# Optimization experiments

Measured on AMD Instinct MI355X. Metric: run time of the kernel, lower is better.

Reference implementation:

```python
import jax, jax.numpy as jnp
import numpy as np

NEG_SLOPE = 0.2  # neg_slope init kwarg


def _segment_softmax(logits, seg, n):
    # numerically stable softmax over edges grouped by destination node
    m = jax.ops.segment_max(logits, seg, num_segments=n)          # [N,H]
    e = jnp.exp(logits - m[seg])                                   # [E,H]
    s = jax.ops.segment_sum(e, seg, num_segments=n)                # [N,H]
    return e / (s[seg] + 1e-16)


def _gat_conv(x, src, dst, W, att_src, att_dst, b, n):
    # PyG GATConv (add_self_loops already applied to src/dst), dropout off (eval)
    H, C = att_src.shape
    h = (x @ W).reshape(n, H, C)                                   # [N,H,C]
    a_src = jnp.einsum('nhc,hc->nh', h, att_src)                   # [N,H]
    a_dst = jnp.einsum('nhc,hc->nh', h, att_dst)                   # [N,H]
    logits = jax.nn.leaky_relu(a_src[src] + a_dst[dst], NEG_SLOPE)  # [E,H]
    alpha = _segment_softmax(logits, dst, n)                       # [E,H]
    msg = h[src] * alpha[:, :, None]                               # [E,H,C]
    out = jax.ops.segment_sum(msg, dst, num_segments=n)            # [N,H,C]
    return out.reshape(n, H * C) + b


def setup_inputs() -> dict:
    key = jax.random.key(0)
    ks = jax.random.split(key, 11)
    NU, NI = 10000, 100000
    N = NU + NI
    E = 1_000_000
    IN, HID, HEADS, OUT = 64, 64, 4, 64
    s = 0.1
    return {
        'edge_index': jax.random.randint(ks[0], (2, E), 0, N, dtype=jnp.int64)
            if jax.config.jax_enable_x64 else jax.random.randint(ks[0], (2, E), 0, N),
        'emb_user': jax.random.normal(ks[1], (NU, IN), jnp.float32) * s,
        'emb_item': jax.random.normal(ks[2], (NI, IN), jnp.float32) * s,
        'W1': jax.random.normal(ks[3], (IN, HEADS * HID), jnp.float32) * s,
        'att_src1': jax.random.normal(ks[4], (HEADS, HID), jnp.float32) * s,
        'att_dst1': jax.random.normal(ks[5], (HEADS, HID), jnp.float32) * s,
        'b1': jnp.zeros((HEADS * HID,), jnp.float32),
        'W2': jax.random.normal(ks[6], (HEADS * HID, OUT), jnp.float32) * s,
        'att_src2': jax.random.normal(ks[7], (1, OUT), jnp.float32) * s,
        'att_dst2': jax.random.normal(ks[8], (1, OUT), jnp.float32) * s,
        'b2': jnp.zeros((OUT,), jnp.float32),
    }


def reference(edge_index, emb_user, emb_item, W1, att_src1, att_dst1, b1,
              W2, att_src2, att_dst2, b2):
    NU = emb_user.shape[0]
    N = NU + emb_item.shape[0]
    x = jnp.concatenate([emb_user, emb_item], axis=0)              # [N,IN]
    # GATConv adds self-loops by default
    loops = jnp.arange(N, dtype=edge_index.dtype)
    src = jnp.concatenate([edge_index[0], loops])
    dst = jnp.concatenate([edge_index[1], loops])
    # dropout layers are identity in eval mode
    x = _gat_conv(x, src, dst, W1, att_src1, att_dst1, b1, N)      # [N,HEADS*HID]
    x = jax.nn.elu(x)
    x = _gat_conv(x, src, dst, W2, att_src2, att_dst2, b2, N)      # [N,OUT]
    return x[:NU], x[NU:]
```

## Files before the change

kernel.cpp:

```cpp
#include <hip/hip_runtime.h>
#include <math.h>


typedef float f32x4 __attribute__((ext_vector_type(4)));
typedef short s16x8 __attribute__((ext_vector_type(8)));

#define CHUNK 4096
#define CAPB 6400
#define PADM 1536
#define CAPT (CAPB + PADM)
#define G2PAD 264
#define SMASK 131071

static __device__ __forceinline__ short f2bf(float f) {
    unsigned u = __builtin_bit_cast(unsigned, f);
    u = (u + 0x7fff + ((u >> 16) & 1)) >> 16;
    return (short)u;
}
static __device__ __forceinline__ float bf2f(unsigned short u) {
    unsigned v = ((unsigned)u) << 16;
    return __builtin_bit_cast(float, v);
}


__global__ __launch_bounds__(256) void bin_kernel(
    const int* __restrict__ ei, int E, int ET, int* __restrict__ acur,
    unsigned long long* __restrict__ staging) {
    __shared__ unsigned long long eds[CHUNK];
    __shared__ int cnt[256], delta[256], cur[256];
    int t = threadIdx.x;
    cnt[t] = 0;
    __syncthreads();
    int c0 = blockIdx.x * CHUNK;
#pragma unroll
    for (int i = t; i < CHUNK; i += 256) {
        int e = c0 + i;
        unsigned long long v = ~0ull;
        if (e < ET) {
            int s, d;
            if (e < E) { s = ei[e]; d = ei[E + e]; } else { s = e - E; d = e - E; }
            v = ((unsigned long long)(unsigned)d << 32) | (unsigned)s;
            atomicAdd(&cnt[d >> 9], 1);
        }
        eds[i] = v;
    }
    __syncthreads();
    if (t < 64) {
        int loc[4], run = 0;
#pragma unroll
        for (int j = 0; j < 4; ++j) { int v = cnt[t * 4 + j]; loc[j] = run; run += v; }
        int inc = run;
#pragma unroll
        for (int off = 1; off < 64; off <<= 1) {
            int u = __shfl_up(inc, off);
            if (t >= off) inc += u;
        }
        int excl = inc - run;
#pragma unroll
        for (int j = 0; j < 4; ++j) {
            int b = t * 4 + j;
            int lofs = excl + loc[j];
            int c = cnt[b];
            int g = (c > 0) ? atomicAdd(&acur[b], c) : 0;
            delta[b] = b * CAPB + g - lofs;
            cur[b] = lofs;
        }
    }
    __syncthreads();
    for (int i = t; i < CHUNK; i += 256) {
        unsigned long long v = eds[i];
        if (v == ~0ull) continue;
        int b = (int)(v >> 32) >> 9;
        int p = atomicAdd(&cur[b], 1);
        int idx = delta[b] + p;
        if (idx < (b + 1) * CAPB) staging[idx] = v;
    }
}

__global__ __launch_bounds__(256) void bucket_scan_kernel(
    const int* __restrict__ acur, int* __restrict__ bbase, int NB) {
    __shared__ int sc[256];
    int t = threadIdx.x;
    int v = 0;
    if (t < NB) {
        int c = min(acur[t], CAPB);
        v = ((c + 3) & ~3) + PADM;
    }
    sc[t] = v;
    __syncthreads();
    if (t == 0) {
        int run = 0;
        for (int i = 0; i < NB; ++i) { int x = sc[i]; sc[i] = run; run += x; }
    }
    __syncthreads();
    if (t < NB) bbase[t] = sc[t];
}

__global__ __launch_bounds__(256) void bucket_build_kernel(
    const unsigned long long* __restrict__ staging, const int* __restrict__ acur,
    const int* __restrict__ bbase, const float* __restrict__ as1e,
    const float* __restrict__ ad1e, int* __restrict__ offs, int* __restrict__ ends,
    int* __restrict__ csr, int* __restrict__ dstA, float* __restrict__ wts1T,
    int N, int ETp, int NB) {
    __shared__ int src_s[CAPT];
    __shared__ unsigned short ln_s[CAPT];
    __shared__ float adl[512 * 8];
    __shared__ int cnt[512];
    __shared__ int lofs[512];
    __shared__ int tot4_s;
    int b = blockIdx.x;
    int t = threadIdx.x;
    int n0 = b << 9;
    int nn = min(512, N - n0);
    int tot = min(acur[b], CAPB);
    for (int i = t; i < nn * 8; i += 256) adl[i] = ad1e[(size_t)n0 * 8 + i];
    for (int i = t; i < 512; i += 256) cnt[i] = 0;
    for (int i = t; i < CAPT; i += 256) src_s[i] = -1;
    __syncthreads();
    const unsigned long long* sp = staging + (size_t)b * CAPB;
    for (int i = t; i < tot; i += 256)
        atomicAdd(&cnt[(int)(sp[i] >> 32) - n0], 1);
    __syncthreads();
    if (t < 64) {
        int loc[8];
        int run = 0;
#pragma unroll
        for (int j = 0; j < 8; ++j) {
            int v = (cnt[t * 8 + j] + 3) & ~3;
            loc[j] = run;
            run += v;
        }
        int inc = run;
#pragma unroll
        for (int off = 1; off < 64; off <<= 1) {
            int u = __shfl_up(inc, off);
            if (t >= off) inc += u;
        }
        int excl = inc - run;
#pragma unroll
        for (int j = 0; j < 8; ++j) lofs[t * 8 + j] = excl + loc[j];
        if (t == 63) tot4_s = inc;
    }
    __syncthreads();
    int base = bbase[b];
    int tot4 = tot4_s;
    for (int i = t; i < nn; i += 256) {
        int beg = base + lofs[i];
        offs[n0 + i] = beg;
        ends[n0 + i] = beg + ((cnt[i] + 3) & ~3);
    }
    if (b == NB - 1 && t == 0) offs[N] = base + tot4;
    __syncthreads();
    for (int i = t; i < 512; i += 256) cnt[i] = 0;
    __syncthreads();
    for (int i = t; i < tot; i += 256) {
        unsigned long long v = sp[i];
        int s = (int)(v & 0xffffffffu);
        int ln = (int)(v >> 32) - n0;
        int p = lofs[ln] + atomicAdd(&cnt[ln], 1);
        src_s[p] = s;
        ln_s[p] = (unsigned short)ln;
    }
    __syncthreads();
    for (int i = t; i < tot4; i += 256) {
        int s = src_s[i];
        if (s < 0) {
            csr[base + i] = 0;
            dstA[base + i] = -1;
            wts1T[(size_t)0 * ETp + base + i] = 0.f;
            wts1T[(size_t)1 * ETp + base + i] = 0.f;
            wts1T[(size_t)2 * ETp + base + i] = 0.f;
            wts1T[(size_t)3 * ETp + base + i] = 0.f;
        } else {
            int ln = ln_s[i];
            csr[base + i] = s;
            dstA[base + i] = n0 + ln;
            const float4* ap = reinterpret_cast<const float4*>(as1e + (size_t)s * 8);
            float4 a0 = ap[0], a1 = ap[1];
            const float* dl = adl + ln * 8;
            float wA, wB;
            wA = a0.x * dl[0]; wB = a0.y * dl[1];
            wts1T[(size_t)0 * ETp + base + i] = (wA >= 1.f) ? wA : wB;
            wA = a0.z * dl[2]; wB = a0.w * dl[3];
            wts1T[(size_t)1 * ETp + base + i] = (wA >= 1.f) ? wA : wB;
            wA = a1.x * dl[4]; wB = a1.y * dl[5];
            wts1T[(size_t)2 * ETp + base + i] = (wA >= 1.f) ? wA : wB;
            wA = a1.z * dl[6]; wB = a1.w * dl[7];
            wts1T[(size_t)3 * ETp + base + i] = (wA >= 1.f) ? wA : wB;
        }
    }
}

__global__ void edge_w2_kernel(const int* __restrict__ csr,
                               const int* __restrict__ dstA,
                               const float* __restrict__ as2e,
                               const float* __restrict__ ad2e,
                               float* __restrict__ wts2, int ETp, int N) {
    int p = blockIdx.x * blockDim.x + threadIdx.x;
    if (p >= ETp) return;
    int d = dstA[p];
    int s = csr[p];
    if ((unsigned)d >= (unsigned)N || (unsigned)s >= (unsigned)N) {
        wts2[p] = 0.f;
        return;
    }
    float2 ae = *reinterpret_cast<const float2*>(as2e + (size_t)s * 2);
    float2 de = *reinterpret_cast<const float2*>(ad2e + (size_t)d * 2);
    float wA = ae.x * de.x, wB = ae.y * de.y;
    wts2[p] = (wA >= 1.f) ? wA : wB;
}

__global__ void prep_attv_kernel(const float* __restrict__ W1,
                                 const float* __restrict__ attS1,
                                 const float* __restrict__ attD1,
                                 const float* __restrict__ W2,
                                 const float* __restrict__ attS2,
                                 const float* __restrict__ attD2,
                                 float* __restrict__ attv1s, float* __restrict__ attv1d,
                                 float* __restrict__ attv2s, float* __restrict__ attv2d) {
    int t = threadIdx.x;
    {
        int k = t >> 2, h = t & 3;
        float ss = 0.f, sd = 0.f;
        for (int c = 0; c < 64; ++c) {
            float w = W1[k * 256 + h * 64 + c];
            ss += w * attS1[h * 64 + c];
            sd += w * attD1[h * 64 + c];
        }
        attv1s[k * 4 + h] = ss;
        attv1d[k * 4 + h] = sd;
    }
    {
        float ss = 0.f, sd = 0.f;
        for (int c = 0; c < 64; ++c) {
            float w = W2[t * 64 + c];
            ss += w * attS2[c];
            sd += w * attD2[c];
        }
        attv2s[t] = ss;
        attv2d[t] = sd;
    }
}

__global__ __launch_bounds__(256) void cast_att_kernel(
    const float* __restrict__ xu, const float* __restrict__ xi, int NU, int N,
    const float* __restrict__ attv1s, const float* __restrict__ attv1d,
    unsigned short* __restrict__ xb, float* __restrict__ as1e,
    float* __restrict__ ad1e) {
    int t = threadIdx.x;
    int wv = t >> 6, l = t & 63, l15 = l & 15, lg = l >> 4;

    s16x8 Bfr[2];
#pragma unroll
    for (int ks = 0; ks < 2; ++ks) {
        s16x8 f;
#pragma unroll
        for (int j = 0; j < 8; ++j) {
            int k = ks * 32 + lg * 8 + j;
            float v = 0.f;
            if (l15 < 4) v = attv1s[k * 4 + l15];
            else if (l15 < 8) v = attv1d[k * 4 + (l15 - 4)];
            f[j] = f2bf(v);
        }
        Bfr[ks] = f;
    }

    int ntile = (N + 15) >> 4;
    int wid = blockIdx.x * 4 + wv;
    int stride = gridDim.x * 4;
    for (int tile = wid; tile < ntile; tile += stride) {
        int rbase = tile * 16;
        int arow = rbase + l15;
        bool valid = (arow < N);
        if (!valid) arow = N - 1;
        const float* xp = (arow < NU) ? (xu + (size_t)arow * 64)
                                      : (xi + (size_t)(arow - NU) * 64);
        s16x8 Afr[2];
#pragma unroll
        for (int ks = 0; ks < 2; ++ks) {
            const float4* p = reinterpret_cast<const float4*>(xp + ks * 32 + lg * 8);
            float4 v0 = p[0];
            float4 v1 = p[1];
            s16x8 f;
            f[0] = f2bf(v0.x); f[1] = f2bf(v0.y); f[2] = f2bf(v0.z); f[3] = f2bf(v0.w);
            f[4] = f2bf(v1.x); f[5] = f2bf(v1.y); f[6] = f2bf(v1.z); f[7] = f2bf(v1.w);
            Afr[ks] = f;
            if (valid)
                *reinterpret_cast<s16x8*>(xb + (size_t)arow * 64 + ks * 32 + lg * 8) = f;
        }
        f32x4 acc = (f32x4){0.f, 0.f, 0.f, 0.f};
        acc = __builtin_amdgcn_mfma_f32_16x16x32_bf16(Afr[0], Bfr[0], acc, 0, 0, 0);
        acc = __builtin_amdgcn_mfma_f32_16x16x32_bf16(Afr[1], Bfr[1], acc, 0, 0, 0);
        if (l15 < 8) {
            float* dst = (l15 < 4) ? as1e : ad1e;
            int h = l15 & 3;
#pragma unroll
            for (int i = 0; i < 4; ++i) {
                int r = rbase + lg * 4 + i;
                if (r < N) {
                    float s = acc[i];
                    dst[(size_t)r * 8 + h * 2 + 0] = __expf(s);
                    dst[(size_t)r * 8 + h * 2 + 1] = __expf(0.2f * s);
                }
            }
        }
    }
}

__global__ __launch_bounds__(256) void agg1_kernel(
    const unsigned short* __restrict__ xb, const float* __restrict__ wts1T,
    const int* __restrict__ offs, const int* __restrict__ ends,
    const int* __restrict__ csr, unsigned short* __restrict__ yb, int N, int ETp) {
    int wv = threadIdx.x >> 6, lane = threadIdx.x & 63;
    int n = __builtin_amdgcn_readfirstlane(blockIdx.x * 4 + wv);
    if (n >= N) return;
    int h = lane >> 4, c4 = (lane & 15) * 4;
    int beg = offs[n], end = ends[n];
    const float* wp = wts1T + (size_t)h * ETp;
    float ss = 0.f, a0 = 0.f, a1 = 0.f, a2 = 0.f, a3 = 0.f;

    f32x4 w0, w1, w2;
    ushort4 r0[4], r1[4], r2[4];

    if (end - beg <= 64) {
        int ci = beg + lane;
        if (ci >= end) ci = beg;
        int csrv = csr[ci] & SMASK;

#define A1F_LOAD(W, R, O)                                                         \
    {                                                                             \
        W = *reinterpret_cast<const f32x4*>(wp + (O));                            \
        _Pragma("unroll") for (int j = 0; j < 4; ++j) {                           \
            int sj = __shfl(csrv, (O) - beg + j);                                 \
            R[j] = *reinterpret_cast<const ushort4*>(xb + (size_t)sj * 64 + c4);  \
        }                                                                         \
    }
#define A1_PROC(W, R)                                                            \
    {                                                                            \
        _Pragma("unroll") for (int j = 0; j < 4; ++j) {                          \
            float w = W[j];                                                      \
            ss += w;                                                             \
            a0 += w * bf2f(R[j].x);                                              \
            a1 += w * bf2f(R[j].y);                                              \
            a2 += w * bf2f(R[j].z);                                              \
            a3 += w * bf2f(R[j].w);                                              \
        }                                                                        \
    }
        A1F_LOAD(w0, r0, beg)
        if (beg + 4 < end) {
            A1F_LOAD(w1, r1, beg + 4)
            int o = beg;
            while (true) {
                if (o + 8 < end) A1F_LOAD(w2, r2, o + 8)
                A1_PROC(w0, r0)
                o += 4; if (o >= end) break;
                if (o + 8 < end) A1F_LOAD(w0, r0, o + 8)
                A1_PROC(w1, r1)
                o += 4; if (o >= end) break;
                if (o + 8 < end) A1F_LOAD(w1, r1, o + 8)
                A1_PROC(w2, r2)
                o += 4; if (o >= end) break;
            }
        } else {
            A1_PROC(w0, r0)
        }
#undef A1F_LOAD
    } else {
#define A1_LOAD(W, R, O)                                                          \
    {                                                                             \
        W = *reinterpret_cast<const f32x4*>(wp + (O));                            \
        _Pragma("unroll") for (int j = 0; j < 4; ++j) {                           \
            int sj = __builtin_amdgcn_readfirstlane(csr[(O) + j]) & SMASK;        \
            R[j] = *reinterpret_cast<const ushort4*>(xb + (size_t)sj * 64 + c4);  \
        }                                                                         \
    }
        A1_LOAD(w0, r0, beg)
        A1_LOAD(w1, r1, beg + 4)
        int o = beg;
        while (true) {
            if (o + 8 < end) A1_LOAD(w2, r2, o + 8)
            A1_PROC(w0, r0)
            o += 4; if (o >= end) break;
            if (o + 8 < end) A1_LOAD(w0, r0, o + 8)
            A1_PROC(w1, r1)
            o += 4; if (o >= end) break;
            if (o + 8 < end) A1_LOAD(w1, r1, o + 8)
            A1_PROC(w2, r2)
            o += 4; if (o >= end) break;
        }
#undef A1_LOAD
#undef A1_PROC
    }
    float inv = 1.f / (ss + 1e-16f);
    ushort4 ov;
    ov.x = (unsigned short)f2bf(a0 * inv);
    ov.y = (unsigned short)f2bf(a1 * inv);
    ov.z = (unsigned short)f2bf(a2 * inv);
    ov.w = (unsigned short)f2bf(a3 * inv);
    *reinterpret_cast<ushort4*>(yb + (size_t)n * 256 + h * 64 + c4) = ov;
}

__global__ __launch_bounds__(256) void gemm_mid_mfma(
    const unsigned short* __restrict__ yb, int N, const float* __restrict__ W1,
    const float* __restrict__ b1, const float* __restrict__ attv2s,
    const float* __restrict__ attv2d, unsigned short* __restrict__ x2,
    float* __restrict__ as2e, float* __restrict__ ad2e) {
    __shared__ float part_s[16][4];
    __shared__ float part_d[16][4];
    int t = threadIdx.x;
    int wv = t >> 6;
    int l = t & 63;
    int l15 = l & 15;
    int lg = l >> 4;

    s16x8 Bfr[4][2];
#pragma unroll
    for (int c = 0; c < 4; ++c)
#pragma unroll
        for (int ks = 0; ks < 2; ++ks) {
            s16x8 f;
#pragma unroll
            for (int j = 0; j < 8; ++j)
                f[j] = f2bf(W1[(size_t)(ks * 32 + lg * 8 + j) * 256 + (wv * 4 + c) * 16 + l15]);
            Bfr[c][ks] = f;
        }
    float bv[4], avs[4], avd[4];
#pragma unroll
    for (int c = 0; c < 4; ++c) {
        int col = (wv * 4 + c) * 16 + l15;
        bv[c] = b1[col];
        avs[c] = attv2s[col];
        avd[c] = attv2d[col];
    }

    int ntile = (N + 15) >> 4;
    for (int tile = blockIdx.x; tile < ntile; tile += gridDim.x) {
        int rbase = tile * 16;
        int arow = rbase + l15;
        if (arow >= N) arow = N - 1;
        const unsigned short* yp = yb + (size_t)arow * 256 + wv * 64;
        s16x8 Afr0 = *reinterpret_cast<const s16x8*>(yp + lg * 8);
        s16x8 Afr1 = *reinterpret_cast<const s16x8*>(yp + 32 + lg * 8);
        f32x4 acc[4];
#pragma unroll
        for (int c = 0; c < 4; ++c) acc[c] = (f32x4){0.f, 0.f, 0.f, 0.f};
#pragma unroll
        for (int c = 0; c < 4; ++c) {
            acc[c] = __builtin_amdgcn_mfma_f32_16x16x32_bf16(Afr0, Bfr[c][0], acc[c], 0, 0, 0);
            acc[c] = __builtin_amdgcn_mfma_f32_16x16x32_bf16(Afr1, Bfr[c][1], acc[c], 0, 0, 0);
        }
        int r0 = rbase + lg * 4;
        float rs[4] = {0.f, 0.f, 0.f, 0.f};
        float rd[4] = {0.f, 0.f, 0.f, 0.f};
#pragma unroll
        for (int c = 0; c < 4; ++c) {
            int col = (wv * 4 + c) * 16 + l15;
#pragma unroll
            for (int i = 0; i < 4; ++i) {
                float v = acc[c][i] + bv[c];
                v = (v > 0.f) ? v : __expf(v) - 1.f;
                rs[i] += v * avs[c];
                rd[i] += v * avd[c];
                int r = r0 + i;
                if (r < N)
                    x2[(size_t)r * 256 + col] = (unsigned short)f2bf(v);
            }
        }
#pragma unroll
        for (int i = 0; i < 4; ++i) {
#pragma unroll
            for (int msk = 8; msk; msk >>= 1) {
                rs[i] += __shfl_xor(rs[i], msk);
                rd[i] += __shfl_xor(rd[i], msk);
            }
            if (l15 == 0) {
                part_s[lg * 4 + i][wv] = rs[i];
                part_d[lg * 4 + i][wv] = rd[i];
            }
        }
        __syncthreads();
        if (t < 16) {
            int r = rbase + t;
            if (r < N) {
                float s = part_s[t][0] + part_s[t][1] + part_s[t][2] + part_s[t][3];
                float d = part_d[t][0] + part_d[t][1] + part_d[t][2] + part_d[t][3];
                as2e[(size_t)r * 2 + 0] = __expf(s);
                as2e[(size_t)r * 2 + 1] = __expf(0.2f * s);
                ad2e[(size_t)r * 2 + 0] = __expf(d);
                ad2e[(size_t)r * 2 + 1] = __expf(0.2f * d);
            }
        }
        __syncthreads();
    }
}

__global__ __launch_bounds__(256) void gemm2_mfma(
    const unsigned short* __restrict__ x2, int N, const float* __restrict__ W2,
    unsigned short* __restrict__ h2) {
    __shared__ unsigned short at[16 * G2PAD];
    int t = threadIdx.x;
    int wv = t >> 6;
    int l = t & 63;
    int l15 = l & 15;
    int lg = l >> 4;

    s16x8 Bfr[8];
#pragma unroll
    for (int ks = 0; ks < 8; ++ks) {
        s16x8 f;
#pragma unroll
        for (int j = 0; j < 8; ++j)
            f[j] = f2bf(W2[(size_t)(ks * 32 + lg * 8 + j) * 64 + wv * 16 + l15]);
        Bfr[ks] = f;
    }

    int ntile = (N + 15) >> 4;
    for (int tile = blockIdx.x; tile < ntile; tile += gridDim.x) {
        int rbase = tile * 16;
        __syncthreads();
#pragma unroll
        for (int k = 0; k < 2; ++k) {
            int i = t * 2 + k;
            int row = i >> 5, c8 = i & 31;
            int r = rbase + row;
            if (r >= N) r = N - 1;
            *reinterpret_cast<uint4*>(at + row * G2PAD + c8 * 8) =
                *reinterpret_cast<const uint4*>(x2 + (size_t)r * 256 + c8 * 8);
        }
        __syncthreads();
        f32x4 acc = (f32x4){0.f, 0.f, 0.f, 0.f};
#pragma unroll
        for (int ks = 0; ks < 8; ++ks) {
            s16x8 Afr = *reinterpret_cast<const s16x8*>(at + l15 * G2PAD + ks * 32 + lg * 8);
            acc = __builtin_amdgcn_mfma_f32_16x16x32_bf16(Afr, Bfr[ks], acc, 0, 0, 0);
        }
        int r0 = rbase + lg * 4;
#pragma unroll
        for (int i = 0; i < 4; ++i) {
            int r = r0 + i;
            if (r < N)
                h2[(size_t)r * 64 + wv * 16 + l15] = (unsigned short)f2bf(acc[i]);
        }
    }
}

__global__ __launch_bounds__(256) void agg2_kernel(
    const unsigned short* __restrict__ h2, const float* __restrict__ wts2,
    const int* __restrict__ offs, const int* __restrict__ ends,
    const int* __restrict__ csr, const float* __restrict__ b2,
    float* __restrict__ out, int N) {
    int wv = threadIdx.x >> 6, lane = threadIdx.x & 63;
    int n = __builtin_amdgcn_readfirstlane(blockIdx.x * 4 + wv);
    if (n >= N) return;
    int beg = offs[n], end = ends[n];
    float ss = 0.f, acc = 0.f;

    f32x4 w0, w1, w2;
    unsigned short r0[4], r1[4], r2[4];

    if (end - beg <= 64) {
        int ci = beg + lane;
        if (ci >= end) ci = beg;
        int csrv = csr[ci] & SMASK;

#define A2F_LOAD(W, R, O)                                                  \
    {                                                                      \
        W = *reinterpret_cast<const f32x4*>(wts2 + (O));                   \
        _Pragma("unroll") for (int j = 0; j < 4; ++j) {                    \
            int sj = __shfl(csrv, (O) - beg + j);                          \
            R[j] = h2[(size_t)sj * 64 + lane];                             \
        }                                                                  \
    }
#define A2_PROC(W, R)                                                      \
    {                                                                      \
        _Pragma("unroll") for (int j = 0; j < 4; ++j) {                    \
            float w = W[j];                                                \
            ss += w;                                                       \
            acc += w * bf2f(R[j]);                                         \
        }                                                                  \
    }
        A2F_LOAD(w0, r0, beg)
        if (beg + 4 < end) {
            A2F_LOAD(w1, r1, beg + 4)
            int o = beg;
            while (true) {
                if (o + 8 < end) A2F_LOAD(w2, r2, o + 8)
                A2_PROC(w0, r0)
                o += 4; if (o >= end) break;
                if (o + 8 < end) A2F_LOAD(w0, r0, o + 8)
                A2_PROC(w1, r1)
                o += 4; if (o >= end) break;
                if (o + 8 < end) A2F_LOAD(w1, r1, o + 8)
                A2_PROC(w2, r2)
                o += 4; if (o >= end) break;
            }
        } else {
            A2_PROC(w0, r0)
        }
#undef A2F_LOAD
    } else {
#define A2_LOAD(W, R, O)                                                   \
    {                                                                      \
        W = *reinterpret_cast<const f32x4*>(wts2 + (O));                   \
        _Pragma("unroll") for (int j = 0; j < 4; ++j) {                    \
            int sj = __builtin_amdgcn_readfirstlane(csr[(O) + j]) & SMASK; \
            R[j] = h2[(size_t)sj * 64 + lane];                             \
        }                                                                  \
    }
        A2_LOAD(w0, r0, beg)
        A2_LOAD(w1, r1, beg + 4)
        int o = beg;
        while (true) {
            if (o + 8 < end) A2_LOAD(w2, r2, o + 8)
            A2_PROC(w0, r0)
            o += 4; if (o >= end) break;
            if (o + 8 < end) A2_LOAD(w0, r0, o + 8)
            A2_PROC(w1, r1)
            o += 4; if (o >= end) break;
            if (o + 8 < end) A2_LOAD(w1, r1, o + 8)
            A2_PROC(w2, r2)
            o += 4; if (o >= end) break;
        }
#undef A2_LOAD
#undef A2_PROC
    }
    out[(size_t)n * 64 + lane] = acc / (ss + 1e-16f) + b2[lane];
}


extern "C" void kernel_launch(void* const* d_in, const int* in_sizes, int n_in,
                              void* d_out, int out_size, void* d_ws, size_t ws_size,
                              hipStream_t stream) {
    const int* ei = (const int*)d_in[0];
    const float* xu = (const float*)d_in[1];
    const float* xi = (const float*)d_in[2];
    const float* W1 = (const float*)d_in[3];
    const float* attS1 = (const float*)d_in[4];
    const float* attD1 = (const float*)d_in[5];
    const float* b1 = (const float*)d_in[6];
    const float* W2 = (const float*)d_in[7];
    const float* attS2 = (const float*)d_in[8];
    const float* attD2 = (const float*)d_in[9];
    const float* b2 = (const float*)d_in[10];
    float* out = (float*)d_out;

    const int E = in_sizes[0] / 2;
    const int NU = in_sizes[1] / 64;
    const int NI = in_sizes[2] / 64;
    const int N = NU + NI;
    const int ET = E + N;
    const int NB = (N + 511) >> 9;
    const int ETp = NB * CAPT;

    char* p = (char*)d_ws;
    auto carve = [&](size_t bytes) {
        void* r = (void*)p;
        p += (bytes + 255) & ~(size_t)255;
        return r;
    };
    unsigned short* xb = (unsigned short*)carve((size_t)N * 64 * 2);
    unsigned short* yb = (unsigned short*)carve((size_t)N * 256 * 2);
    unsigned short* x2 = (unsigned short*)carve((size_t)N * 256 * 2);
    float* as1e = (float*)carve((size_t)N * 8 * 4);
    float* ad1e = (float*)carve((size_t)N * 8 * 4);
    float* as2e = (float*)carve((size_t)N * 2 * 4);
    float* ad2e = (float*)carve((size_t)N * 2 * 4);
    float* attv1s = (float*)carve(256 * 4);
    float* attv1d = (float*)carve(256 * 4);
    float* attv2s = (float*)carve(256 * 4);
    float* attv2d = (float*)carve(256 * 4);
    int* offs = (int*)carve((size_t)(N + 1) * 4);
    int* ends = (int*)carve((size_t)N * 4);
    int* csr = (int*)carve((size_t)ETp * 4);
    int* dstA = (int*)carve((size_t)ETp * 4);
    float* wts1T = (float*)carve((size_t)4 * ETp * 4);
    float* wts2 = (float*)carve(((size_t)ETp + 16) * 4);
    int* acur = (int*)carve((size_t)NB * 4);
    int* bbase = (int*)carve((size_t)NB * 4);
    unsigned long long* staging = (unsigned long long*)yb;
    unsigned short* h2 = yb;

    prep_attv_kernel<<<1, 256, 0, stream>>>(W1, attS1, attD1, W2, attS2, attD2,
                                            attv1s, attv1d, attv2s, attv2d);
    {
        int ntile = (N + 15) >> 4;
        cast_att_kernel<<<(ntile + 3) / 4, 256, 0, stream>>>(
            xu, xi, NU, N, attv1s, attv1d, xb, as1e, ad1e);
    }

    hipMemsetAsync(acur, 0, (size_t)NB * 4, stream);
    {
        int grid = (ET + CHUNK - 1) / CHUNK;
        bin_kernel<<<grid, 256, 0, stream>>>(ei, E, ET, acur, staging);
    }
    bucket_scan_kernel<<<1, 256, 0, stream>>>(acur, bbase, NB);
    bucket_build_kernel<<<NB, 256, 0, stream>>>(staging, acur, bbase, as1e, ad1e,
                                                offs, ends, csr, dstA, wts1T,
                                                N, ETp, NB);

    agg1_kernel<<<(N + 3) / 4, 256, 0, stream>>>(xb, wts1T, offs, ends, csr, yb, N, ETp);
    gemm_mid_mfma<<<1024, 256, 0, stream>>>(yb, N, W1, b1, attv2s, attv2d, x2, as2e, ad2e);

    {
        int grid = (ETp + 255) / 256;
        edge_w2_kernel<<<grid, 256, 0, stream>>>(csr, dstA, as2e, ad2e, wts2, ETp, N);
    }
    gemm2_mfma<<<1024, 256, 0, stream>>>(x2, N, W2, h2);
    agg2_kernel<<<(N + 3) / 4, 256, 0, stream>>>(h2, wts2, offs, ends, csr, b2, out, N);
}
```

Before: 232.8 us.

## Halve bucket size, fold bucket scan into build, fuse edge weights into gemm2

Buckets now cover 256 destination nodes instead of 512, giving about 430 buckets with smaller per-bucket capacity and padding. Each build block redoes the bucket-base prefix scan itself, which removes the single-block scan kernel. The layer-2 edge-weight computation moves into a grid-stride tail of gemm2, removing another launch. Together these cut launch count and shared-memory footprint and should raise occupancy in bucket_build. The costs are redundant scan work in every build block and a higher risk of dropping edges if a bucket's in-degree exceeds the smaller cap.

```diff
diff --git a/kernel.cpp b/kernel.cpp
--- a/kernel.cpp
+++ b/kernel.cpp
@@ -6,9 +6,10 @@
 typedef short s16x8 __attribute__((ext_vector_type(8)));
 
 #define CHUNK 4096
-#define CAPB 6400
-#define PADM 1536
-#define CAPT (CAPB + PADM)
+#define CAPB 3328
+#define PADM 768
+#define CAPT 4096
+#define NBMAX 512
 #define G2PAD 264
 #define SMASK 131071
 
@@ -27,9 +28,9 @@
     const int* __restrict__ ei, int E, int ET, int* __restrict__ acur,
     unsigned long long* __restrict__ staging) {
     __shared__ unsigned long long eds[CHUNK];
-    __shared__ int cnt[256], delta[256], cur[256];
+    __shared__ int cnt[NBMAX], delta[NBMAX], cur[NBMAX];
     int t = threadIdx.x;
-    cnt[t] = 0;
+    for (int i = t; i < NBMAX; i += 256) cnt[i] = 0;
     __syncthreads();
     int c0 = blockIdx.x * CHUNK;
 #pragma unroll
@@ -40,15 +41,15 @@
             int s, d;
             if (e < E) { s = ei[e]; d = ei[E + e]; } else { s = e - E; d = e - E; }
             v = ((unsigned long long)(unsigned)d << 32) | (unsigned)s;
-            atomicAdd(&cnt[d >> 9], 1);
+            atomicAdd(&cnt[d >> 8], 1);
         }
         eds[i] = v;
     }
     __syncthreads();
     if (t < 64) {
-        int loc[4], run = 0;
-#pragma unroll
-        for (int j = 0; j < 4; ++j) { int v = cnt[t * 4 + j]; loc[j] = run; run += v; }
+        int loc[8], run = 0;
+#pragma unroll
+        for (int j = 0; j < 8; ++j) { int v = cnt[t * 8 + j]; loc[j] = run; run += v; }
         int inc = run;
 #pragma unroll
         for (int off = 1; off < 64; off <<= 1) {
@@ -57,8 +58,8 @@
         }
         int excl = inc - run;
 #pragma unroll
-        for (int j = 0; j < 4; ++j) {
-            int b = t * 4 + j;
+        for (int j = 0; j < 8; ++j) {
+            int b = t * 8 + j;
             int lofs = excl + loc[j];
             int c = cnt[b];
             int g = (c > 0) ? atomicAdd(&acur[b], c) : 0;
@@ -70,63 +71,64 @@
     for (int i = t; i < CHUNK; i += 256) {
         unsigned long long v = eds[i];
         if (v == ~0ull) continue;
-        int b = (int)(v >> 32) >> 9;
+        int b = (int)(v >> 32) >> 8;
         int p = atomicAdd(&cur[b], 1);
         int idx = delta[b] + p;
         if (idx < (b + 1) * CAPB) staging[idx] = v;
     }
 }
 
-__global__ __launch_bounds__(256) void bucket_scan_kernel(
-    const int* __restrict__ acur, int* __restrict__ bbase, int NB) {
-    __shared__ int sc[256];
-    int t = threadIdx.x;
-    int v = 0;
-    if (t < NB) {
-        int c = min(acur[t], CAPB);
-        v = ((c + 3) & ~3) + PADM;
-    }
-    sc[t] = v;
-    __syncthreads();
-    if (t == 0) {
-        int run = 0;
-        for (int i = 0; i < NB; ++i) { int x = sc[i]; sc[i] = run; run += x; }
-    }
-    __syncthreads();
-    if (t < NB) bbase[t] = sc[t];
-}
-
 __global__ __launch_bounds__(256) void bucket_build_kernel(
     const unsigned long long* __restrict__ staging, const int* __restrict__ acur,
-    const int* __restrict__ bbase, const float* __restrict__ as1e,
-    const float* __restrict__ ad1e, int* __restrict__ offs, int* __restrict__ ends,
-    int* __restrict__ csr, int* __restrict__ dstA, float* __restrict__ wts1T,
+    const float* __restrict__ as1e, const float* __restrict__ ad1e,
+    int* __restrict__ offs, int* __restrict__ ends, int* __restrict__ csr,
+    int* __restrict__ dstA, float* __restrict__ wts1T,
     int N, int ETp, int NB) {
     __shared__ int src_s[CAPT];
     __shared__ unsigned short ln_s[CAPT];
-    __shared__ float adl[512 * 8];
-    __shared__ int cnt[512];
-    __shared__ int lofs[512];
+    __shared__ float adl[256 * 8];
+    __shared__ int cnt[256];
+    __shared__ int lofs[256];
+    __shared__ int ab[NBMAX];
     __shared__ int tot4_s;
     int b = blockIdx.x;
     int t = threadIdx.x;
-    int n0 = b << 9;
-    int nn = min(512, N - n0);
+    int n0 = b << 8;
+    int nn = min(256, N - n0);
     int tot = min(acur[b], CAPB);
+
+    for (int i = t; i < NBMAX; i += 256)
+        ab[i] = (i < NB) ? (((min(acur[i], CAPB) + 3) & ~3) + PADM) : 0;
     for (int i = t; i < nn * 8; i += 256) adl[i] = ad1e[(size_t)n0 * 8 + i];
-    for (int i = t; i < 512; i += 256) cnt[i] = 0;
+    if (t < 256) cnt[t] = 0;
     for (int i = t; i < CAPT; i += 256) src_s[i] = -1;
     __syncthreads();
+    if (t < 64) {
+        int loc[8], run = 0;
+#pragma unroll
+        for (int j = 0; j < 8; ++j) { int v = ab[t * 8 + j]; loc[j] = run; run += v; }
+        int inc = run;
+#pragma unroll
+        for (int off = 1; off < 64; off <<= 1) {
+            int u = __shfl_up(inc, off);
+            if (t >= off) inc += u;
+        }
+        int excl = inc - run;
+#pragma unroll
+        for (int j = 0; j < 8; ++j) ab[t * 8 + j] = excl + loc[j];
+    }
+    __syncthreads();
+    int base = ab[b];
+
     const unsigned long long* sp = staging + (size_t)b * CAPB;
     for (int i = t; i < tot; i += 256)
         atomicAdd(&cnt[(int)(sp[i] >> 32) - n0], 1);
     __syncthreads();
     if (t < 64) {
-        int loc[8];
-        int run = 0;
-#pragma unroll
-        for (int j = 0; j < 8; ++j) {
-            int v = (cnt[t * 8 + j] + 3) & ~3;
+        int loc[4], run = 0;
+#pragma unroll
+        for (int j = 0; j < 4; ++j) {
+            int v = (cnt[t * 4 + j] + 3) & ~3;
             loc[j] = run;
             run += v;
         }
@@ -138,11 +140,10 @@
         }
         int excl = inc - run;
 #pragma unroll
-        for (int j = 0; j < 8; ++j) lofs[t * 8 + j] = excl + loc[j];
+        for (int j = 0; j < 4; ++j) lofs[t * 4 + j] = excl + loc[j];
         if (t == 63) tot4_s = inc;
     }
     __syncthreads();
-    int base = bbase[b];
     int tot4 = tot4_s;
     for (int i = t; i < nn; i += 256) {
         int beg = base + lofs[i];
@@ -151,7 +152,7 @@
     }
     if (b == NB - 1 && t == 0) offs[N] = base + tot4;
     __syncthreads();
-    for (int i = t; i < 512; i += 256) cnt[i] = 0;
+    if (t < 256) cnt[t] = 0;
     __syncthreads();
     for (int i = t; i < tot; i += 256) {
         unsigned long long v = sp[i];
@@ -191,25 +192,6 @@
     }
 }
 
-__global__ void edge_w2_kernel(const int* __restrict__ csr,
-                               const int* __restrict__ dstA,
-                               const float* __restrict__ as2e,
-                               const float* __restrict__ ad2e,
-                               float* __restrict__ wts2, int ETp, int N) {
-    int p = blockIdx.x * blockDim.x + threadIdx.x;
-    if (p >= ETp) return;
-    int d = dstA[p];
-    int s = csr[p];
-    if ((unsigned)d >= (unsigned)N || (unsigned)s >= (unsigned)N) {
-        wts2[p] = 0.f;
-        return;
-    }
-    float2 ae = *reinterpret_cast<const float2*>(as2e + (size_t)s * 2);
-    float2 de = *reinterpret_cast<const float2*>(ad2e + (size_t)d * 2);
-    float wA = ae.x * de.x, wB = ae.y * de.y;
-    wts2[p] = (wA >= 1.f) ? wA : wB;
-}
-
 __global__ void prep_attv_kernel(const float* __restrict__ W1,
                                  const float* __restrict__ attS1,
                                  const float* __restrict__ attD1,
@@ -496,7 +478,9 @@
 
 __global__ __launch_bounds__(256) void gemm2_mfma(
     const unsigned short* __restrict__ x2, int N, const float* __restrict__ W2,
-    unsigned short* __restrict__ h2) {
+    unsigned short* __restrict__ h2, const int* __restrict__ csr,
+    const int* __restrict__ dstA, const float* __restrict__ as2e,
+    const float* __restrict__ ad2e, float* __restrict__ wts2, int ETp) {
     __shared__ unsigned short at[16 * G2PAD];
     int t = threadIdx.x;
     int wv = t >> 6;
@@ -541,6 +525,18 @@
             if (r < N)
                 h2[(size_t)r * 64 + wv * 16 + l15] = (unsigned short)f2bf(acc[i]);
         }
+    }
+    for (int p = blockIdx.x * 256 + t; p < ETp; p += gridDim.x * 256) {
+        int d = dstA[p];
+        int s = csr[p];
+        float w = 0.f;
+        if ((unsigned)d < (unsigned)N && (unsigned)s < (unsigned)N) {
+            float2 ae = *reinterpret_cast<const float2*>(as2e + (size_t)s * 2);
+            float2 de = *reinterpret_cast<const float2*>(ad2e + (size_t)d * 2);
+            float wA = ae.x * de.x, wB = ae.y * de.y;
+            w = (wA >= 1.f) ? wA : wB;
+        }
+        wts2[p] = w;
     }
 }
 
@@ -649,7 +645,7 @@
     const int NI = in_sizes[2] / 64;
     const int N = NU + NI;
     const int ET = E + N;
-    const int NB = (N + 511) >> 9;
+    const int NB = (N + 255) >> 8;
     const int ETp = NB * CAPT;
 
     char* p = (char*)d_ws;
@@ -675,8 +671,7 @@
     int* dstA = (int*)carve((size_t)ETp * 4);
     float* wts1T = (float*)carve((size_t)4 * ETp * 4);
     float* wts2 = (float*)carve(((size_t)ETp + 16) * 4);
-    int* acur = (int*)carve((size_t)NB * 4);
-    int* bbase = (int*)carve((size_t)NB * 4);
+    int* acur = (int*)carve((size_t)NBMAX * 4);
     unsigned long long* staging = (unsigned long long*)yb;
     unsigned short* h2 = yb;
 
@@ -688,23 +683,19 @@
             xu, xi, NU, N, attv1s, attv1d, xb, as1e, ad1e);
     }
 
-    hipMemsetAsync(acur, 0, (size_t)NB * 4, stream);
+    hipMemsetAsync(acur, 0, (size_t)NBMAX * 4, stream);
     {
         int grid = (ET + CHUNK - 1) / CHUNK;
         bin_kernel<<<grid, 256, 0, stream>>>(ei, E, ET, acur, staging);
     }
-    bucket_scan_kernel<<<1, 256, 0, stream>>>(acur, bbase, NB);
-    bucket_build_kernel<<<NB, 256, 0, stream>>>(staging, acur, bbase, as1e, ad1e,
+    bucket_build_kernel<<<NB, 256, 0, stream>>>(staging, acur, as1e, ad1e,
                                                 offs, ends, csr, dstA, wts1T,
                                                 N, ETp, NB);
 
     agg1_kernel<<<(N + 3) / 4, 256, 0, stream>>>(xb, wts1T, offs, ends, csr, yb, N, ETp);
     gemm_mid_mfma<<<1024, 256, 0, stream>>>(yb, N, W1, b1, attv2s, attv2d, x2, as2e, ad2e);
 
-    {
-        int grid = (ETp + 255) / 256;
-        edge_w2_kernel<<<grid, 256, 0, stream>>>(csr, dstA, as2e, ad2e, wts2, ETp, N);
-    }
-    gemm2_mfma<<<1024, 256, 0, stream>>>(x2, N, W2, h2);
+    gemm2_mfma<<<1024, 256, 0, stream>>>(x2, N, W2, h2, csr, dstA, as2e, ad2e,
+                                         wts2, ETp);
     agg2_kernel<<<(N + 3) / 4, 256, 0, stream>>>(h2, wts2, offs, ends, csr, b2, out, N);
 }
```

Result: slower. 240.8 us (+3.5%).
